# Performance work log

Measured on AMD Instinct MI355X. Metric: run time of the kernel, lower is better.

Reference implementation:

```python
import jax, jax.numpy as jnp
import numpy as np

B, C, OC, K, HW = 32, 256, 256, 3, 56
M, G = 2, 2
GAP = max(16, C // 16)          # input_gap = 16
MO = M * OC                      # fc1 out channels = 512
FC2_OUT = OC * C * K * K         # 589824
PER = FC2_OUT // MO              # per-group out channels of fc2 = 1152


def setup_inputs() -> dict:
    key = jax.random.key(0)
    ks = jax.random.split(key, 6)
    x = jax.random.normal(ks[0], (B, C, HW, HW), dtype=jnp.float32)
    reduce_w = jax.random.normal(ks[1], (GAP, C), dtype=jnp.float32) / np.sqrt(C)
    reduce_b = jnp.zeros((GAP,), dtype=jnp.float32)
    fc1_w = jax.random.normal(ks[2], (MO, GAP), dtype=jnp.float32) / np.sqrt(GAP)
    # fc2: grouped 1x1 conv, groups=G*OC=512, 1 in-channel per group -> weight (FC2_OUT,)
    fc2_w = jax.random.normal(ks[3], (FC2_OUT,), dtype=jnp.float32)
    fc2_b = jax.random.normal(ks[4], (FC2_OUT,), dtype=jnp.float32) * 0.01
    return {"x": x, "reduce_w": reduce_w, "reduce_b": reduce_b,
            "fc1_w": fc1_w, "fc2_w": fc2_w, "fc2_b": fc2_b}


def reference(x, reduce_w, reduce_b, fc1_w, fc2_w, fc2_b):
    b, c, h, w = x.shape
    # global average pool -> (b, C)
    gap = x.mean(axis=(2, 3))
    # reduce: 1x1 conv on 1x1 map == linear
    g = gap @ reduce_w.T + reduce_b                      # (b, GAP)
    # fc1 (no bias) + sigmoid
    a = jax.nn.sigmoid(g @ fc1_w.T)                      # (b, MO)
    # fc2: grouped 1x1 conv with 1 input channel per group:
    # out[:, g*PER + j] = a[:, g] * fc2_w[g*PER + j] + fc2_b[g*PER + j]
    wk = a[:, :, None] * fc2_w.reshape(MO, PER)[None] + fc2_b.reshape(MO, PER)[None]
    wk = wk.reshape(b * OC, c, K, K)                     # per-sample conv kernels
    pad = K // 2
    y = jax.lax.conv_general_dilated(
        x.reshape(1, b * c, h, w), wk,
        window_strides=(1, 1), padding=[(pad, pad), (pad, pad)],
        feature_group_count=b,
        dimension_numbers=("NCHW", "OIHW", "NCHW"))
    return y.reshape(b, OC, y.shape[2], y.shape[3])
```

## Files before the change

### kernel.cpp

```cpp
#include <hip/hip_runtime.h>
#include <hip/hip_bf16.h>
#include <stdint.h>

#define NB   32
#define NC   256
#define NOC  256
#define HWD  56
#define NPIX 3136
#define PW   58
#define PPIX 3364
#define KTOT 2304
#define MOD  512
#define GAPD 16

#define XBT_BYTES ((size_t)NB * PPIX * NC * 2)
#define WA_BYTES  ((size_t)NB * NOC * KTOT * 2)

typedef __bf16 bf16x8 __attribute__((ext_vector_type(8)));
typedef float  f32x4  __attribute__((ext_vector_type(4)));
typedef unsigned short u16x8 __attribute__((ext_vector_type(8)));

__device__ __forceinline__ unsigned short f2bf(float f) {
    union { float f; unsigned int u; } v; v.f = f;
    unsigned int u = v.u;
    return (unsigned short)((u + 0x7FFFu + ((u >> 16) & 1u)) >> 16);
}

__global__ void se_kernel(const float* __restrict__ gap,
                          const float* __restrict__ rw, const float* __restrict__ rb,
                          const float* __restrict__ f1w, float* __restrict__ a2) {
    __shared__ float sgap[NB * NC];
    __shared__ float sg[NB * GAPD];
    int t = threadIdx.x;
    #pragma unroll
    for (int i = 0; i < 16; ++i) sgap[i * 512 + t] = gap[i * 512 + t];
    __syncthreads();
    {
        int b = t >> 4, tt = t & 15;
        float s = rb[tt];
        for (int c = 0; c < NC; ++c) s += sgap[b * NC + c] * rw[tt * NC + c];
        sg[b * GAPD + tt] = s;
    }
    __syncthreads();
    for (int i = 0; i < 32; ++i) {
        int o = i * 512 + t;
        int b = o >> 9, m = o & 511;
        float s = 0.f;
        #pragma unroll
        for (int tt = 0; tt < GAPD; ++tt) s += sg[b * GAPD + tt] * f1w[m * GAPD + tt];
        a2[o] = 1.0f / (1.0f + __expf(-s));
    }
}

__global__ void wk_kernel(const float* __restrict__ a2,
                          const float* __restrict__ f2w, const float* __restrict__ f2b,
                          unsigned short* __restrict__ wa) {
    int oc = blockIdx.x, b = blockIdx.y, c = threadIdx.x;
    float a0 = a2[b * MOD + 2 * oc];
    float a1 = a2[b * MOD + 2 * oc + 1];
    unsigned short* dst = wa + (size_t)(b * NOC + oc) * KTOT;
    const float* wsrc = f2w + (size_t)oc * KTOT;
    const float* bsrc = f2b + (size_t)oc * KTOT;
    #pragma unroll
    for (int s = 0; s < 9; ++s) {
        int rem = c * 9 + s;
        float a = (rem >= 1152) ? a1 : a0;
        float v = a * wsrc[rem] + bsrc[rem];
        dst[s * NC + c] = f2bf(v);
    }
}

__global__ void halo_kernel(unsigned short* __restrict__ xbt) {
    int b = blockIdx.x, t = threadIdx.x;
    unsigned short* xb = xbt + (size_t)b * PPIX * NC;
    u16x8 z = {};
    for (int i = t; i < 3712; i += 256) {
        int r = (i >= 1856) ? 1 : 0;
        int c = i - r * 1856;
        int pix = r * (57 * 58) + (c >> 5);
        *(u16x8*)(xb + (size_t)pix * NC + (c & 31) * 8) = z;
    }
    for (int i = t; i < 3584; i += 256) {
        int row = 1 + (i >> 6);
        int side = (i >> 5) & 1;
        int pix = row * PW + side * 57;
        *(u16x8*)(xb + (size_t)pix * NC + (i & 31) * 8) = z;
    }
}

__global__ void xpose_kernel(const float* __restrict__ x, unsigned short* __restrict__ xbt,
                             float* __restrict__ gap) {
    __shared__ unsigned short tile[NC][57];
    int py = blockIdx.x, b = blockIdx.y, t = threadIdx.x;
    const float* xs = x + (size_t)b * NC * NPIX + py * HWD;
    for (int i = 0; i < 56; ++i) {
        int lin = i * 256 + t;
        int c = lin / 56, px = lin % 56;
        tile[c][px] = f2bf(xs[(size_t)c * NPIX + px]);
    }
    __syncthreads();
    {
        float s = 0.f;
        #pragma unroll
        for (int px = 0; px < 56; ++px) {
            union { unsigned int u; float f; } cv;
            cv.u = ((unsigned int)tile[t][px]) << 16;
            s += cv.f;
        }
        atomicAdd(&gap[b * NC + t], s * (1.0f / NPIX));
    }
    int cch = t & 31, pg = t >> 5;
    for (int i = 0; i < 7; ++i) {
        int px = pg * 7 + i;
        u16x8 v;
        #pragma unroll
        for (int j = 0; j < 8; ++j) v[j] = tile[cch * 8 + j][px];
        *(u16x8*)(xbt + ((size_t)b * PPIX + (size_t)(1 + py) * PW + 1 + px) * NC + cch * 8) = v;
    }
}

#define SLICE_BYTES 32768
#define B_OFF 16384

#define PWAIT(N) do { asm volatile("s_waitcnt vmcnt(" #N ")" ::: "memory"); \
    __builtin_amdgcn_s_barrier(); __builtin_amdgcn_sched_barrier(0); } while (0)

__global__ __launch_bounds__(512, 2) void conv_gemm(
    const unsigned short* __restrict__ wa,
    const unsigned short* __restrict__ xbt,
    float* __restrict__ out)
{
    __shared__ __attribute__((aligned(16))) char lds[4 * SLICE_BYTES];

    const int bid = blockIdx.x;
    const int wg  = (bid & 7) * 52 + (bid >> 3);
    const int nt  = wg % 13, b = wg / 13;

    const int t = threadIdx.x;
    const int w = t >> 6, l = t & 63;
    const int wm = w >> 2, wn = w & 3;

    const unsigned short* waB = wa + (size_t)b * NOC * KTOT;
    const unsigned short* xbB = xbt + (size_t)b * PPIX * NC;

    const int srow = l >> 2;
    const int sq   = (l & 3) ^ ((l >> 3) & 3);
    const unsigned short* pA0 = waB + (size_t)(w * 16 + srow) * KTOT + sq * 8;
    const unsigned short* pA1 = waB + (size_t)((w + 8) * 16 + srow) * KTOT + sq * 8;
    int pg0 = nt * 256 + (2 * w) * 16 + srow;     if (pg0 > NPIX - 1) pg0 = NPIX - 1;
    int pg1 = nt * 256 + (2 * w + 1) * 16 + srow; if (pg1 > NPIX - 1) pg1 = NPIX - 1;
    const int py0 = pg0 / 56, px0 = pg0 - py0 * 56;
    const int py1 = pg1 / 56, px1 = pg1 - py1 * 56;
    const unsigned short* pB0 = xbB + (size_t)((py0 + 1) * PW + (px0 + 1)) * NC + sq * 8;
    const unsigned short* pB1 = xbB + (size_t)((py1 + 1) * PW + (px1 + 1)) * NC + sq * 8;

    f32x4 acc[8][4] = {};

    auto issue = [&](int tp) {
        const int ss = tp & 3;
        char* sb = lds + ss * SLICE_BYTES;
        const int koff = tp * 32;
        const int s9 = tp >> 3;
        const int dy = s9 / 3, dx = s9 - dy * 3;
        const int bsh = ((dy - 1) * PW + (dx - 1)) * NC + (tp & 7) * 32;
        __builtin_amdgcn_global_load_lds(
            (const __attribute__((address_space(1))) void*)(pA0 + koff),
            (__attribute__((address_space(3))) void*)(sb + w * 1024), 16, 0, 0);
        __builtin_amdgcn_global_load_lds(
            (const __attribute__((address_space(1))) void*)(pA1 + koff),
            (__attribute__((address_space(3))) void*)(sb + (w + 8) * 1024), 16, 0, 0);
        __builtin_amdgcn_global_load_lds(
            (const __attribute__((address_space(1))) void*)(pB0 + bsh),
            (__attribute__((address_space(3))) void*)(sb + B_OFF + (2 * w) * 1024), 16, 0, 0);
        __builtin_amdgcn_global_load_lds(
            (const __attribute__((address_space(1))) void*)(pB1 + bsh),
            (__attribute__((address_space(3))) void*)(sb + B_OFF + (2 * w + 1) * 1024), 16, 0, 0);
    };

    const int physq16 = (((l >> 4) ^ ((l >> 1) & 3)) << 4);
    const int arow = (l & 15) << 6;

    auto compute = [&](int p) {
        const char* sb = lds + (p & 3) * SLICE_BYTES;
        bf16x8 af[8], bfr[4];
        #pragma unroll
        for (int i = 0; i < 8; ++i)
            af[i] = *(const bf16x8*)(sb + wm * 8192 + i * 1024 + arow + physq16);
        #pragma unroll
        for (int j = 0; j < 4; ++j)
            bfr[j] = *(const bf16x8*)(sb + B_OFF + wn * 4096 + j * 1024 + arow + physq16);
        __builtin_amdgcn_s_setprio(1);
        #pragma unroll
        for (int i = 0; i < 8; ++i)
            #pragma unroll
            for (int j = 0; j < 4; ++j)
                acc[i][j] = __builtin_amdgcn_mfma_f32_16x16x32_bf16(af[i], bfr[j], acc[i][j], 0, 0, 0);
        __builtin_amdgcn_s_setprio(0);
    };

    issue(0); issue(1);
    #pragma unroll 4
    for (int p = 0; p < 68; ++p) { issue(p + 2); PWAIT(8); compute(p); }
    issue(70); PWAIT(8); compute(68);
    issue(71); PWAIT(8); compute(69);
    PWAIT(4);  compute(70);
    PWAIT(0);  compute(71);

    const int ocb = wm * 128 + ((l >> 4) << 2);
    const int pxb = nt * 256 + wn * 64 + (l & 15);
    #pragma unroll
    for (int i = 0; i < 8; ++i) {
        #pragma unroll
        for (int j = 0; j < 4; ++j) {
            int p = pxb + j * 16;
            if (p < NPIX) {
                float* o = out + ((size_t)(b * NOC + ocb + i * 16)) * NPIX + p;
                o[0]        = acc[i][j][0];
                o[NPIX]     = acc[i][j][1];
                o[2 * NPIX] = acc[i][j][2];
                o[3 * NPIX] = acc[i][j][3];
            }
        }
    }
}

extern "C" void kernel_launch(void* const* d_in, const int* in_sizes, int n_in,
                              void* d_out, int out_size, void* d_ws, size_t ws_size,
                              hipStream_t stream) {
    (void)in_sizes; (void)n_in; (void)out_size; (void)ws_size;
    const float* x   = (const float*)d_in[0];
    const float* rw  = (const float*)d_in[1];
    const float* rb  = (const float*)d_in[2];
    const float* f1w = (const float*)d_in[3];
    const float* f2w = (const float*)d_in[4];
    const float* f2b = (const float*)d_in[5];
    float* out = (float*)d_out;

    char* wsb = (char*)d_ws;
    unsigned short* xbt = (unsigned short*)wsb;
    unsigned short* wa  = (unsigned short*)(wsb + XBT_BYTES);
    float* gap = (float*)(wsb + XBT_BYTES + WA_BYTES);
    float* a2  = (float*)(wsb + XBT_BYTES + WA_BYTES + (size_t)NB * NC * 4);

    hipMemsetAsync(gap, 0, (size_t)NB * NC * 4, stream);
    halo_kernel<<<dim3(32), 256, 0, stream>>>(xbt);
    xpose_kernel<<<dim3(56, 32), 256, 0, stream>>>(x, xbt, gap);
    se_kernel<<<dim3(1), 512, 0, stream>>>(gap, rw, rb, f1w, a2);
    wk_kernel<<<dim3(256, 32), 256, 0, stream>>>(a2, f2w, f2b, wa);
    conv_gemm<<<dim3(416), 512, 0, stream>>>(wa, xbt, out);
}
```

Measured before the change: 214.6 us.

## Use 4-wave 128x128 warp tiles in conv GEMM and vectorize prep kernels

The conv GEMM block goes from 8 waves to 4 waves, and each wave now computes a 128x128 sub-tile (8x8 MFMA accumulators) instead of 128x64. This cuts LDS fragment reads per MFMA and doubles the global-to-LDS loads each thread issues. Separately, the transpose kernel reads x with float4 loads into a tile padded to stride 59. The wk kernel stages fc2 weights and biases through shared memory with float4 loads instead of strided scalar reads. The trade-off is heavy register pressure from 256 accumulator floats and half the waves per block available to hide latency.

Result: slower. 223.5 us (+4.2%).

```diff
diff --git a/kernel.cpp b/kernel.cpp
--- a/kernel.cpp
+++ b/kernel.cpp
@@ -55,17 +55,29 @@
 __global__ void wk_kernel(const float* __restrict__ a2,
                           const float* __restrict__ f2w, const float* __restrict__ f2b,
                           unsigned short* __restrict__ wa) {
+    __shared__ float sw[KTOT];
+    __shared__ float sbv[KTOT];
     int oc = blockIdx.x, b = blockIdx.y, c = threadIdx.x;
+    const float4* wsrc = (const float4*)(f2w + (size_t)oc * KTOT);
+    const float4* bsrc = (const float4*)(f2b + (size_t)oc * KTOT);
+    #pragma unroll
+    for (int i = 0; i < 3; ++i) {
+        int idx = i * 256 + c;
+        if (idx < 576) {
+            float4 wv = wsrc[idx], bv = bsrc[idx];
+            ((float4*)sw)[idx] = wv;
+            ((float4*)sbv)[idx] = bv;
+        }
+    }
     float a0 = a2[b * MOD + 2 * oc];
     float a1 = a2[b * MOD + 2 * oc + 1];
+    __syncthreads();
     unsigned short* dst = wa + (size_t)(b * NOC + oc) * KTOT;
-    const float* wsrc = f2w + (size_t)oc * KTOT;
-    const float* bsrc = f2b + (size_t)oc * KTOT;
     #pragma unroll
     for (int s = 0; s < 9; ++s) {
         int rem = c * 9 + s;
         float a = (rem >= 1152) ? a1 : a0;
-        float v = a * wsrc[rem] + bsrc[rem];
+        float v = a * sw[rem] + sbv[rem];
         dst[s * NC + c] = f2bf(v);
     }
 }
@@ -88,15 +100,23 @@
     }
 }
 
+#define TSTR 59
 __global__ void xpose_kernel(const float* __restrict__ x, unsigned short* __restrict__ xbt,
                              float* __restrict__ gap) {
-    __shared__ unsigned short tile[NC][57];
+    __shared__ unsigned short tile[NC * TSTR];
     int py = blockIdx.x, b = blockIdx.y, t = threadIdx.x;
+    int wv = t >> 6, l = t & 63;
     const float* xs = x + (size_t)b * NC * NPIX + py * HWD;
-    for (int i = 0; i < 56; ++i) {
-        int lin = i * 256 + t;
-        int c = lin / 56, px = lin % 56;
-        tile[c][px] = f2bf(xs[(size_t)c * NPIX + px]);
+    int q = l & 15;
+    int rb4 = l >> 4;
+    #pragma unroll
+    for (int it = 0; it < 16; ++it) {
+        int c = wv * 64 + it * 4 + rb4;
+        if (q < 14) {
+            float4 v = *(const float4*)(xs + (size_t)c * NPIX + q * 4);
+            unsigned short* tr = tile + c * TSTR + q * 4;
+            tr[0] = f2bf(v.x); tr[1] = f2bf(v.y); tr[2] = f2bf(v.z); tr[3] = f2bf(v.w);
+        }
     }
     __syncthreads();
     {
@@ -104,7 +124,7 @@
         #pragma unroll
         for (int px = 0; px < 56; ++px) {
             union { unsigned int u; float f; } cv;
-            cv.u = ((unsigned int)tile[t][px]) << 16;
+            cv.u = ((unsigned int)tile[t * TSTR + px]) << 16;
             s += cv.f;
         }
         atomicAdd(&gap[b * NC + t], s * (1.0f / NPIX));
@@ -114,7 +134,7 @@
         int px = pg * 7 + i;
         u16x8 v;
         #pragma unroll
-        for (int j = 0; j < 8; ++j) v[j] = tile[cch * 8 + j][px];
+        for (int j = 0; j < 8; ++j) v[j] = tile[(cch * 8 + j) * TSTR + px];
         *(u16x8*)(xbt + ((size_t)b * PPIX + (size_t)(1 + py) * PW + 1 + px) * NC + cch * 8) = v;
     }
 }
@@ -125,7 +145,7 @@
 #define PWAIT(N) do { asm volatile("s_waitcnt vmcnt(" #N ")" ::: "memory"); \
     __builtin_amdgcn_s_barrier(); __builtin_amdgcn_sched_barrier(0); } while (0)
 
-__global__ __launch_bounds__(512, 2) void conv_gemm(
+__global__ __launch_bounds__(256, 1) void conv_gemm(
     const unsigned short* __restrict__ wa,
     const unsigned short* __restrict__ xbt,
     float* __restrict__ out)
@@ -138,43 +158,42 @@
 
     const int t = threadIdx.x;
     const int w = t >> 6, l = t & 63;
-    const int wm = w >> 2, wn = w & 3;
+    const int wm = w >> 1, wn = w & 1;
 
     const unsigned short* waB = wa + (size_t)b * NOC * KTOT;
     const unsigned short* xbB = xbt + (size_t)b * PPIX * NC;
 
     const int srow = l >> 2;
     const int sq   = (l & 3) ^ ((l >> 3) & 3);
-    const unsigned short* pA0 = waB + (size_t)(w * 16 + srow) * KTOT + sq * 8;
-    const unsigned short* pA1 = waB + (size_t)((w + 8) * 16 + srow) * KTOT + sq * 8;
-    int pg0 = nt * 256 + (2 * w) * 16 + srow;     if (pg0 > NPIX - 1) pg0 = NPIX - 1;
-    int pg1 = nt * 256 + (2 * w + 1) * 16 + srow; if (pg1 > NPIX - 1) pg1 = NPIX - 1;
-    const int py0 = pg0 / 56, px0 = pg0 - py0 * 56;
-    const int py1 = pg1 / 56, px1 = pg1 - py1 * 56;
-    const unsigned short* pB0 = xbB + (size_t)((py0 + 1) * PW + (px0 + 1)) * NC + sq * 8;
-    const unsigned short* pB1 = xbB + (size_t)((py1 + 1) * PW + (px1 + 1)) * NC + sq * 8;
-
-    f32x4 acc[8][4] = {};
+    const unsigned short* pA[4];
+    const unsigned short* pB[4];
+    #pragma unroll
+    for (int i = 0; i < 4; ++i) {
+        int m = i * 64 + w * 16 + srow;
+        pA[i] = waB + (size_t)m * KTOT + sq * 8;
+        int pg = nt * 256 + m; if (pg > NPIX - 1) pg = NPIX - 1;
+        int py = pg / 56, px = pg - py * 56;
+        pB[i] = xbB + (size_t)((py + 1) * PW + (px + 1)) * NC + sq * 8;
+    }
+
+    f32x4 acc[8][8] = {};
 
     auto issue = [&](int tp) {
-        const int ss = tp & 3;
-        char* sb = lds + ss * SLICE_BYTES;
+        char* sb = lds + (tp & 3) * SLICE_BYTES;
         const int koff = tp * 32;
         const int s9 = tp >> 3;
         const int dy = s9 / 3, dx = s9 - dy * 3;
         const int bsh = ((dy - 1) * PW + (dx - 1)) * NC + (tp & 7) * 32;
-        __builtin_amdgcn_global_load_lds(
-            (const __attribute__((address_space(1))) void*)(pA0 + koff),
-            (__attribute__((address_space(3))) void*)(sb + w * 1024), 16, 0, 0);
-        __builtin_amdgcn_global_load_lds(
-            (const __attribute__((address_space(1))) void*)(pA1 + koff),
-            (__attribute__((address_space(3))) void*)(sb + (w + 8) * 1024), 16, 0, 0);
-        __builtin_amdgcn_global_load_lds(
-            (const __attribute__((address_space(1))) void*)(pB0 + bsh),
-            (__attribute__((address_space(3))) void*)(sb + B_OFF + (2 * w) * 1024), 16, 0, 0);
-        __builtin_amdgcn_global_load_lds(
-            (const __attribute__((address_space(1))) void*)(pB1 + bsh),
-            (__attribute__((address_space(3))) void*)(sb + B_OFF + (2 * w + 1) * 1024), 16, 0, 0);
+        #pragma unroll
+        for (int i = 0; i < 4; ++i)
+            __builtin_amdgcn_global_load_lds(
+                (const __attribute__((address_space(1))) void*)(pA[i] + koff),
+                (__attribute__((address_space(3))) void*)(sb + (i * 4 + w) * 1024), 16, 0, 0);
+        #pragma unroll
+        for (int i = 0; i < 4; ++i)
+            __builtin_amdgcn_global_load_lds(
+                (const __attribute__((address_space(1))) void*)(pB[i] + bsh),
+                (__attribute__((address_space(3))) void*)(sb + B_OFF + (i * 4 + w) * 1024), 16, 0, 0);
     };
 
     const int physq16 = (((l >> 4) ^ ((l >> 1) & 3)) << 4);
@@ -182,36 +201,36 @@
 
     auto compute = [&](int p) {
         const char* sb = lds + (p & 3) * SLICE_BYTES;
-        bf16x8 af[8], bfr[4];
+        bf16x8 af[8], bfr[8];
         #pragma unroll
         for (int i = 0; i < 8; ++i)
             af[i] = *(const bf16x8*)(sb + wm * 8192 + i * 1024 + arow + physq16);
         #pragma unroll
-        for (int j = 0; j < 4; ++j)
-            bfr[j] = *(const bf16x8*)(sb + B_OFF + wn * 4096 + j * 1024 + arow + physq16);
+        for (int j = 0; j < 8; ++j)
+            bfr[j] = *(const bf16x8*)(sb + B_OFF + wn * 8192 + j * 1024 + arow + physq16);
         __builtin_amdgcn_s_setprio(1);
         #pragma unroll
         for (int i = 0; i < 8; ++i)
             #pragma unroll
-            for (int j = 0; j < 4; ++j)
+            for (int j = 0; j < 8; ++j)
                 acc[i][j] = __builtin_amdgcn_mfma_f32_16x16x32_bf16(af[i], bfr[j], acc[i][j], 0, 0, 0);
         __builtin_amdgcn_s_setprio(0);
     };
 
     issue(0); issue(1);
     #pragma unroll 4
-    for (int p = 0; p < 68; ++p) { issue(p + 2); PWAIT(8); compute(p); }
-    issue(70); PWAIT(8); compute(68);
-    issue(71); PWAIT(8); compute(69);
-    PWAIT(4);  compute(70);
+    for (int p = 0; p < 68; ++p) { issue(p + 2); PWAIT(16); compute(p); }
+    issue(70); PWAIT(16); compute(68);
+    issue(71); PWAIT(16); compute(69);
+    PWAIT(8);  compute(70);
     PWAIT(0);  compute(71);
 
     const int ocb = wm * 128 + ((l >> 4) << 2);
-    const int pxb = nt * 256 + wn * 64 + (l & 15);
+    const int pxb = nt * 256 + wn * 128 + (l & 15);
     #pragma unroll
     for (int i = 0; i < 8; ++i) {
         #pragma unroll
-        for (int j = 0; j < 4; ++j) {
+        for (int j = 0; j < 8; ++j) {
             int p = pxb + j * 16;
             if (p < NPIX) {
                 float* o = out + ((size_t)(b * NOC + ocb + i * 16)) * NPIX + p;
@@ -247,5 +266,5 @@
     xpose_kernel<<<dim3(56, 32), 256, 0, stream>>>(x, xbt, gap);
     se_kernel<<<dim3(1), 512, 0, stream>>>(gap, rw, rb, f1w, a2);
     wk_kernel<<<dim3(256, 32), 256, 0, stream>>>(a2, f2w, f2b, wa);
-    conv_gemm<<<dim3(416), 512, 0, stream>>>(wa, xbt, out);
-}
+    conv_gemm<<<dim3(416), 256, 0, stream>>>(wa, xbt, out);
+}
```
